# Kernel optimization log

Measured on AMD Instinct MI355X. Metric: run time of the kernel, lower is better.

## Reference

```python
import jax, jax.numpy as jnp
import numpy as np

D = 1024
N_A = 4096
N_V = 4096


def setup_inputs() -> dict:
    key = jax.random.key(0)
    ks = jax.random.split(key, 6)
    s = 1.0 / np.sqrt(D)  # like torch Linear default init scale
    return {
        "inputs_a": jax.random.normal(ks[0], (N_A, D), dtype=jnp.float32),
        "inputs_v": jax.random.normal(ks[1], (N_V, D), dtype=jnp.float32),
        "W_Ba": jax.random.uniform(ks[2], (D, D), jnp.float32, -s, s),
        "W_Aa": jax.random.uniform(ks[3], (D, D), jnp.float32, -s, s),
        "W_Bv": jax.random.uniform(ks[4], (D, D), jnp.float32, -s, s),
        "W_Av": jax.random.uniform(ks[5], (D, D), jnp.float32, -s, s),
    }


def reference(inputs_a, inputs_v, W_Ba, W_Aa, W_Bv, W_Av):
    # torch Linear: y = x @ W.T ; weights stored [out, in]
    a_a = inputs_a @ W_Aa.T                      # [N_a, D]
    b_a = inputs_a @ W_Ba.T                      # [N_a, D]
    a_v = inputs_v @ W_Av.T                      # [N_v, D]
    b_v = inputs_v @ W_Bv.T                      # [N_v, D]
    scores = b_a @ a_v.T                         # [N_a, N_v]
    alpha_av = jax.nn.softmax(scores, axis=1)    # softmax over N_v
    att_avv = alpha_av @ b_v                     # [N_a, D]
    att_vaa = alpha_av.T @ a_a                   # [N_v, D]
    feature_map_a = att_avv + inputs_a
    feature_map_v = att_vaa + inputs_v
    return feature_map_a, feature_map_v
```

## Files before the change

### kernel.cpp

```cpp
#include <hip/hip_runtime.h>
#include <stdint.h>

#define D_DIM 1024
#define NA_DIM 4096
#define NV_DIM 4096

typedef __bf16 bf16_t;
typedef __bf16 bf16x8 __attribute__((ext_vector_type(8)));
typedef float f32x4 __attribute__((ext_vector_type(4)));

__device__ __forceinline__ void gload_lds16(const void* g, void* lds) {
  __builtin_amdgcn_global_load_lds(
      (const __attribute__((address_space(1))) unsigned int*)g,
      (__attribute__((address_space(3))) unsigned int*)lds, 16, 0, 0);
}

#define VMW(N) asm volatile("s_waitcnt vmcnt(" #N ")" ::: "memory")
#define LKW(N) asm volatile("s_waitcnt lgkmcnt(" #N ")" ::: "memory")
#define SB0() __builtin_amdgcn_sched_barrier(0)
#define BAR() asm volatile("s_barrier" ::: "memory")

__device__ __forceinline__ void gemm256_pl(const bf16_t* __restrict__ A,
                                           const bf16_t* __restrict__ B,
                                           int K, int kb, int klen, int bm, int bn,
                                           bf16_t* lds, f32x4 acc[8][4]) {
  const int tid = threadIdx.x;
  const int lane = tid & 63;
  const int wid = tid >> 6;
  const int wm = wid >> 2;
  const int wn = wid & 3;
  const int frow = lane & 15;
  const int hi = lane >> 4;
  const int k0e = ((hi ^ (frow & 7)) << 3);

  const int sr = (wid << 4) + (lane >> 3);
  const int sc = (((lane & 7) ^ (lane >> 3)) << 3);
  const bf16_t* pAs = A + (size_t)(bm + sr) * K + kb + sc;
  const bf16_t* pBs = B + (size_t)(bn + sr) * K + kb + sc;
  const int dstW = wid << 10;

  const int aBase = (wm << 13) + frow * 64 + k0e;
  const int bBase = 16384 + ((wn >> 1) << 13) + ((wn & 1) << 12) + frow * 64 + k0e;

#define STG_A(kt, h, bufb) do { \
    const bf16_t* s_ = pAs + (size_t)((h) * 128) * K + (size_t)(kt) * 64; \
    bf16_t* d_ = lds + (bufb) * 32768 + (h) * 8192 + dstW; \
    gload_lds16(s_, d_); gload_lds16(s_ + (size_t)8 * K, d_ + 512); } while (0)
#define STG_B(kt, h, bufb) do { \
    const bf16_t* s_ = pBs + (size_t)((h) * 128) * K + (size_t)(kt) * 64; \
    bf16_t* d_ = lds + (bufb) * 32768 + 16384 + (h) * 8192 + dstW; \
    gload_lds16(s_, d_); gload_lds16(s_ + (size_t)8 * K, d_ + 512); } while (0)

  bf16x8 aF[2][4];
  bf16x8 bF[4][2];

#define READ_A(S, Q, BUFB) do { const bf16_t* Lb_ = lds + (BUFB) * 32768; \
    aF[S][0] = *(const bf16x8*)&Lb_[aBase + (Q) * 2048]; \
    aF[S][1] = *(const bf16x8*)&Lb_[(aBase ^ 32) + (Q) * 2048]; \
    aF[S][2] = *(const bf16x8*)&Lb_[aBase + (Q) * 2048 + 1024]; \
    aF[S][3] = *(const bf16x8*)&Lb_[(aBase ^ 32) + (Q) * 2048 + 1024]; } while (0)
#define READ_B(BUFB) do { const bf16_t* Lb_ = lds + (BUFB) * 32768; \
    _Pragma("unroll") for (int fc = 0; fc < 4; ++fc) { \
      bF[fc][0] = *(const bf16x8*)&Lb_[bBase + fc * 1024]; \
      bF[fc][1] = *(const bf16x8*)&Lb_[(bBase ^ 32) + fc * 1024]; } } while (0)

#define MFMA16(S, Q) do { \
    __builtin_amdgcn_s_setprio(1); \
    _Pragma("unroll") for (int fc = 0; fc < 4; ++fc) { \
      acc[(Q) * 2][fc]     = __builtin_amdgcn_mfma_f32_16x16x32_bf16(aF[S][0], bF[fc][0], acc[(Q) * 2][fc], 0, 0, 0); \
      acc[(Q) * 2][fc]     = __builtin_amdgcn_mfma_f32_16x16x32_bf16(aF[S][1], bF[fc][1], acc[(Q) * 2][fc], 0, 0, 0); \
      acc[(Q) * 2 + 1][fc] = __builtin_amdgcn_mfma_f32_16x16x32_bf16(aF[S][2], bF[fc][0], acc[(Q) * 2 + 1][fc], 0, 0, 0); \
      acc[(Q) * 2 + 1][fc] = __builtin_amdgcn_mfma_f32_16x16x32_bf16(aF[S][3], bF[fc][1], acc[(Q) * 2 + 1][fc], 0, 0, 0); \
    } \
    __builtin_amdgcn_s_setprio(0); } while (0)

#define TILE(P, T) do { \
    const bool mA = ((T) + 1 < NT); \
    const bool mB = ((T) + 2 < NT); \
     \
    READ_B(P); READ_A(0, 0, P); READ_A(1, 1, P); \
    if (mA) STG_A((T) + 1, 0, (P) ^ 1); \
    BAR(); LKW(4); SB0(); MFMA16(0, 0); BAR(); \
     \
    READ_A(0, 2, P); \
    if (mA) STG_A((T) + 1, 1, (P) ^ 1); \
    BAR(); LKW(4); SB0(); MFMA16(1, 1); BAR(); \
     \
    READ_A(1, 3, P); \
    if (mB) STG_B((T) + 2, 0, P); \
    BAR(); LKW(4); SB0(); MFMA16(0, 2); BAR(); \
     \
    if (mB) { STG_B((T) + 2, 1, P); VMW(4); } else { VMW(0); } \
    BAR(); LKW(0); SB0(); MFMA16(1, 3); BAR(); \
  } while (0)

  const int NT = klen >> 6;

  STG_B(0, 0, 0); STG_B(0, 1, 0); STG_A(0, 0, 0); STG_A(0, 1, 0);
  STG_B(1, 0, 1); STG_B(1, 1, 1);
  VMW(4);
  BAR();

  for (int it = 0; it < (NT >> 1); ++it) {
    TILE(0, 2 * it);
    TILE(1, 2 * it + 1);
  }
  VMW(0);
#undef TILE
#undef MFMA16
#undef READ_A
#undef READ_B
#undef STG_A
#undef STG_B
}

template <int BF16OUT>
__device__ __forceinline__ void store256(void* Cv, int ldc, int bm, int bn, f32x4 acc[8][4]) {
  const int lane = threadIdx.x & 63;
  const int wid = threadIdx.x >> 6;
  const int wm = wid >> 2, wn = wid & 3;
  const int frow = lane & 15, hi = lane >> 4;
  const int row0 = bm + wm * 128 + hi * 4;
  const int col0 = bn + wn * 64 + frow;
#pragma unroll
  for (int rf = 0; rf < 8; ++rf)
#pragma unroll
    for (int fc = 0; fc < 4; ++fc)
#pragma unroll
      for (int r = 0; r < 4; ++r) {
        size_t idx = (size_t)(row0 + rf * 16 + r) * ldc + (col0 + fc * 16);
        if constexpr (BF16OUT) ((bf16_t*)Cv)[idx] = (bf16_t)acc[rf][fc][r];
        else ((float*)Cv)[idx] = acc[rf][fc][r];
      }
}

__global__ __launch_bounds__(512, 1) void gemm_proj4(
    const bf16_t* __restrict__ Xa, const bf16_t* __restrict__ Xv,
    const bf16_t* __restrict__ W0, const bf16_t* __restrict__ W1,
    const bf16_t* __restrict__ W2, const bf16_t* __restrict__ W3,
    bf16_t* __restrict__ C0, bf16_t* __restrict__ C1,
    bf16_t* __restrict__ C2, bf16_t* __restrict__ C3) {
  __shared__ bf16_t lds[65536];
  const int z = blockIdx.z;
  const bf16_t* A = (z < 2) ? Xa : Xv;
  const bf16_t* B = (z == 0) ? W0 : (z == 1) ? W1 : (z == 2) ? W2 : W3;
  bf16_t* C = (z == 0) ? C0 : (z == 1) ? C1 : (z == 2) ? C2 : C3;
  f32x4 acc[8][4] = {};
  gemm256_pl(A, B, D_DIM, 0, D_DIM, blockIdx.x * 256, blockIdx.y * 256, lds, acc);
  store256<1>(C, D_DIM, blockIdx.x * 256, blockIdx.y * 256, acc);
}

__global__ __launch_bounds__(512, 1) void gemm_scores(const bf16_t* __restrict__ A,
                                                      const bf16_t* __restrict__ B,
                                                      float* __restrict__ C) {
  __shared__ bf16_t lds[65536];
  f32x4 acc[8][4] = {};
  gemm256_pl(A, B, D_DIM, 0, D_DIM, blockIdx.x * 256, blockIdx.y * 256, lds, acc);
  store256<0>(C, NV_DIM, blockIdx.x * 256, blockIdx.y * 256, acc);
}

__global__ __launch_bounds__(512, 1) void gemm_splitk(
    const bf16_t* __restrict__ alpha, const bf16_t* __restrict__ bvT,
    const bf16_t* __restrict__ alphaT, const bf16_t* __restrict__ aaT,
    float* __restrict__ P) {
  __shared__ bf16_t lds[65536];
  const int z = blockIdx.z;
  const bf16_t* A = (z < 2) ? alpha : alphaT;
  const bf16_t* B = (z < 2) ? bvT : aaT;
  const int kb = (z & 1) * 2048;
  f32x4 acc[8][4] = {};
  gemm256_pl(A, B, 4096, kb, 2048, blockIdx.x * 256, blockIdx.y * 256, lds, acc);
  store256<0>(P + (size_t)z * NA_DIM * D_DIM, D_DIM, blockIdx.x * 256, blockIdx.y * 256, acc);
}

__global__ __launch_bounds__(256) void reduce_splitk(const float* __restrict__ P,
                                                     const float* __restrict__ resA,
                                                     const float* __restrict__ resV,
                                                     float* __restrict__ out) {
  const int g = blockIdx.y;
  const size_t n = (size_t)NA_DIM * D_DIM;
  size_t i = ((size_t)blockIdx.x * 256 + threadIdx.x) * 4;
  const float* p0 = P + (size_t)g * 2 * n;
  const float* p1 = p0 + n;
  const float* r = g ? resV : resA;
  float4 a = *(const float4*)(p0 + i);
  float4 b = *(const float4*)(p1 + i);
  float4 c = *(const float4*)(r + i);
  float4 o = {a.x + b.x + c.x, a.y + b.y + c.y, a.z + b.z + c.z, a.w + b.w + c.w};
  *(float4*)(out + g * n + i) = o;
}

__device__ __forceinline__ void cvt8(const float* in, bf16_t* out, int i) {
  float4 v0 = *(const float4*)(in + i);
  float4 v1 = *(const float4*)(in + i + 4);
  bf16x8 o;
  o[0] = (bf16_t)v0.x; o[1] = (bf16_t)v0.y; o[2] = (bf16_t)v0.z; o[3] = (bf16_t)v0.w;
  o[4] = (bf16_t)v1.x; o[5] = (bf16_t)v1.y; o[6] = (bf16_t)v1.z; o[7] = (bf16_t)v1.w;
  *(bf16x8*)(out + i) = o;
}

__global__ __launch_bounds__(256) void cvt2(const float* __restrict__ inA,
                                            const float* __restrict__ inV,
                                            bf16_t* __restrict__ oA,
                                            bf16_t* __restrict__ oV) {
  const float* in = blockIdx.y ? inV : inA;
  bf16_t* out = blockIdx.y ? oV : oA;
  cvt8(in, out, (blockIdx.x * 256 + threadIdx.x) * 8);
}

__global__ __launch_bounds__(256) void cvt4(const float* __restrict__ i0, const float* __restrict__ i1,
                                            const float* __restrict__ i2, const float* __restrict__ i3,
                                            bf16_t* __restrict__ o0, bf16_t* __restrict__ o1,
                                            bf16_t* __restrict__ o2, bf16_t* __restrict__ o3) {
  const int z = blockIdx.y;
  const float* in = (z == 0) ? i0 : (z == 1) ? i1 : (z == 2) ? i2 : i3;
  bf16_t* out = (z == 0) ? o0 : (z == 1) ? o1 : (z == 2) ? o2 : o3;
  cvt8(in, out, (blockIdx.x * 256 + threadIdx.x) * 8);
}

__global__ __launch_bounds__(256) void softmax_rows(const float* __restrict__ S,
                                                    bf16_t* __restrict__ P) {
  const int row = blockIdx.x;
  const int ncol = 4096;
  const float* s = S + (size_t)row * ncol;
  const int base = threadIdx.x * 16;
  float v[16];
  float4* vp = (float4*)v;
#pragma unroll
  for (int q = 0; q < 4; ++q) vp[q] = *(const float4*)(s + base + q * 4);
  float m = v[0];
#pragma unroll
  for (int q = 1; q < 16; ++q) m = fmaxf(m, v[q]);
  for (int off = 32; off; off >>= 1) m = fmaxf(m, __shfl_xor(m, off));
  __shared__ float sm[4], ss[4];
  const int wid = threadIdx.x >> 6, lane = threadIdx.x & 63;
  if (lane == 0) sm[wid] = m;
  __syncthreads();
  m = fmaxf(fmaxf(sm[0], sm[1]), fmaxf(sm[2], sm[3]));
  float sum = 0.f;
#pragma unroll
  for (int q = 0; q < 16; ++q) { v[q] = __expf(v[q] - m); sum += v[q]; }
  for (int off = 32; off; off >>= 1) sum += __shfl_xor(sum, off);
  if (lane == 0) ss[wid] = sum;
  __syncthreads();
  const float inv = 1.0f / (ss[0] + ss[1] + ss[2] + ss[3]);
  bf16x8 o0, o1;
#pragma unroll
  for (int q = 0; q < 8; ++q) { o0[q] = (bf16_t)(v[q] * inv); o1[q] = (bf16_t)(v[q + 8] * inv); }
  bf16_t* p = P + (size_t)row * ncol + base;
  *(bf16x8*)p = o0;
  *(bf16x8*)(p + 8) = o1;
}

__global__ __launch_bounds__(256) void transpose_bf16(const bf16_t* __restrict__ in,
                                                      bf16_t* __restrict__ out, int R, int C) {
  __shared__ bf16_t t[64][72];
  const int bx = blockIdx.x * 64;
  const int by = blockIdx.y * 64;
  const int tid = threadIdx.x;
  const int c8 = (tid & 7) * 8;
  const int r = tid >> 3;
#pragma unroll
  for (int rr = 0; rr < 64; rr += 32) {
    bf16x8 v = *(const bf16x8*)(in + (size_t)(by + r + rr) * C + bx + c8);
    *(bf16x8*)&t[r + rr][c8] = v;
  }
  __syncthreads();
#pragma unroll
  for (int rr = 0; rr < 64; rr += 32) {
    bf16x8 v;
#pragma unroll
    for (int q = 0; q < 8; ++q) v[q] = t[c8 + q][r + rr];
    *(bf16x8*)(out + (size_t)(bx + r + rr) * R + by + c8) = v;
  }
}

extern "C" void kernel_launch(void* const* d_in, const int* in_sizes, int n_in,
                              void* d_out, int out_size, void* d_ws, size_t ws_size,
                              hipStream_t stream) {
  (void)in_sizes; (void)n_in; (void)out_size; (void)ws_size;
  const float* inA = (const float*)d_in[0];
  const float* inV = (const float*)d_in[1];
  const float* wBa = (const float*)d_in[2];
  const float* wAa = (const float*)d_in[3];
  const float* wBv = (const float*)d_in[4];
  const float* wAv = (const float*)d_in[5];
  float* out = (float*)d_out;

  char* w = (char*)d_ws;
  auto take = [&](size_t bytes) { void* p = (void*)w; w += bytes; return p; };
  const size_t XB = (size_t)NA_DIM * D_DIM * 2;
  const size_t WB = (size_t)D_DIM * D_DIM * 2;
  bf16_t* XaB = (bf16_t*)take(XB);
  bf16_t* XvB = (bf16_t*)take(XB);
  bf16_t* WBaB = (bf16_t*)take(WB);
  bf16_t* WAaB = (bf16_t*)take(WB);
  bf16_t* WBvB = (bf16_t*)take(WB);
  bf16_t* WAvB = (bf16_t*)take(WB);
  bf16_t* b_a = (bf16_t*)take(XB);
  bf16_t* a_v = (bf16_t*)take(XB);
  bf16_t* a_a = (bf16_t*)take(XB);
  bf16_t* b_v = (bf16_t*)take(XB);
  bf16_t* a_aT = (bf16_t*)take(XB);
  bf16_t* b_vT = (bf16_t*)take(XB);
  float* scores = (float*)take((size_t)NA_DIM * NV_DIM * 4);
  bf16_t* alpha = (bf16_t*)take((size_t)NA_DIM * NV_DIM * 2);
  bf16_t* alphaT = (bf16_t*)take((size_t)NA_DIM * NV_DIM * 2);
  float* P = scores;

  cvt2<<<dim3(NA_DIM * D_DIM / 2048, 2), 256, 0, stream>>>(inA, inV, XaB, XvB);
  cvt4<<<dim3(D_DIM * D_DIM / 2048, 4), 256, 0, stream>>>(wBa, wAa, wAv, wBv,
                                                          WBaB, WAaB, WAvB, WBvB);

  gemm_proj4<<<dim3(NA_DIM / 256, D_DIM / 256, 4), 512, 0, stream>>>(
      XaB, XvB, WBaB, WAaB, WAvB, WBvB, b_a, a_a, a_v, b_v);

  gemm_scores<<<dim3(NA_DIM / 256, NV_DIM / 256), 512, 0, stream>>>(b_a, a_v, scores);

  softmax_rows<<<NA_DIM, 256, 0, stream>>>(scores, alpha);

  transpose_bf16<<<dim3(NV_DIM / 64, NA_DIM / 64), 256, 0, stream>>>(alpha, alphaT, NA_DIM, NV_DIM);
  transpose_bf16<<<dim3(D_DIM / 64, NA_DIM / 64), 256, 0, stream>>>(a_a, a_aT, NA_DIM, D_DIM);
  transpose_bf16<<<dim3(D_DIM / 64, NV_DIM / 64), 256, 0, stream>>>(b_v, b_vT, NV_DIM, D_DIM);

  gemm_splitk<<<dim3(NA_DIM / 256, D_DIM / 256, 4), 512, 0, stream>>>(
      alpha, b_vT, alphaT, a_aT, P);
  reduce_splitk<<<dim3(NA_DIM * D_DIM / 1024, 2), 256, 0, stream>>>(P, inA, inV, out);
}
```

Before: 211.6 us.

## Replace hand-scheduled GEMM pipeline with simple double-buffered loop

Removes the hand-interleaved four-phase schedule with barriers, priority hints and sched_barriers in the shared GEMM mainloop. The new loop issues the next tile's A and B loads up front, then reads LDS fragments and runs the MFMAs, with a full wait and barrier at the end of each tile. It leaves instruction scheduling to the compiler and simplifies the code, at the cost of less fine-grained overlap between loads and math.

Measured after the change: 209.7 us. About the same (-0.9%).

```diff
diff --git a/kernel.cpp b/kernel.cpp
--- a/kernel.cpp
+++ b/kernel.cpp
@@ -17,13 +17,12 @@
 
 #define VMW(N) asm volatile("s_waitcnt vmcnt(" #N ")" ::: "memory")
 #define LKW(N) asm volatile("s_waitcnt lgkmcnt(" #N ")" ::: "memory")
-#define SB0() __builtin_amdgcn_sched_barrier(0)
 #define BAR() asm volatile("s_barrier" ::: "memory")
 
-__device__ __forceinline__ void gemm256_pl(const bf16_t* __restrict__ A,
-                                           const bf16_t* __restrict__ B,
-                                           int K, int kb, int klen, int bm, int bn,
-                                           bf16_t* lds, f32x4 acc[8][4]) {
+__device__ __forceinline__ void gemm256_loose(const bf16_t* __restrict__ A,
+                                              const bf16_t* __restrict__ B,
+                                              int K, int kb, int klen, int bm, int bn,
+                                              bf16_t* lds, f32x4 acc[8][4]) {
   const int tid = threadIdx.x;
   const int lane = tid & 63;
   const int wid = tid >> 6;
@@ -51,65 +50,48 @@
     bf16_t* d_ = lds + (bufb) * 32768 + 16384 + (h) * 8192 + dstW; \
     gload_lds16(s_, d_); gload_lds16(s_ + (size_t)8 * K, d_ + 512); } while (0)
 
-  bf16x8 aF[2][4];
-  bf16x8 bF[4][2];
-
-#define READ_A(S, Q, BUFB) do { const bf16_t* Lb_ = lds + (BUFB) * 32768; \
-    aF[S][0] = *(const bf16x8*)&Lb_[aBase + (Q) * 2048]; \
-    aF[S][1] = *(const bf16x8*)&Lb_[(aBase ^ 32) + (Q) * 2048]; \
-    aF[S][2] = *(const bf16x8*)&Lb_[aBase + (Q) * 2048 + 1024]; \
-    aF[S][3] = *(const bf16x8*)&Lb_[(aBase ^ 32) + (Q) * 2048 + 1024]; } while (0)
-#define READ_B(BUFB) do { const bf16_t* Lb_ = lds + (BUFB) * 32768; \
-    _Pragma("unroll") for (int fc = 0; fc < 4; ++fc) { \
-      bF[fc][0] = *(const bf16x8*)&Lb_[bBase + fc * 1024]; \
-      bF[fc][1] = *(const bf16x8*)&Lb_[(bBase ^ 32) + fc * 1024]; } } while (0)
-
-#define MFMA16(S, Q) do { \
-    __builtin_amdgcn_s_setprio(1); \
-    _Pragma("unroll") for (int fc = 0; fc < 4; ++fc) { \
-      acc[(Q) * 2][fc]     = __builtin_amdgcn_mfma_f32_16x16x32_bf16(aF[S][0], bF[fc][0], acc[(Q) * 2][fc], 0, 0, 0); \
-      acc[(Q) * 2][fc]     = __builtin_amdgcn_mfma_f32_16x16x32_bf16(aF[S][1], bF[fc][1], acc[(Q) * 2][fc], 0, 0, 0); \
-      acc[(Q) * 2 + 1][fc] = __builtin_amdgcn_mfma_f32_16x16x32_bf16(aF[S][2], bF[fc][0], acc[(Q) * 2 + 1][fc], 0, 0, 0); \
-      acc[(Q) * 2 + 1][fc] = __builtin_amdgcn_mfma_f32_16x16x32_bf16(aF[S][3], bF[fc][1], acc[(Q) * 2 + 1][fc], 0, 0, 0); \
+#define MFMA(a, b, c) __builtin_amdgcn_mfma_f32_16x16x32_bf16((a), (b), (c), 0, 0, 0)
+
+#define TILE(P, T) do { \
+    if ((T) + 1 < NT) { \
+      STG_A((T) + 1, 0, (P) ^ 1); STG_A((T) + 1, 1, (P) ^ 1); \
+      STG_B((T) + 1, 0, (P) ^ 1); STG_B((T) + 1, 1, (P) ^ 1); \
     } \
-    __builtin_amdgcn_s_setprio(0); } while (0)
-
-#define TILE(P, T) do { \
-    const bool mA = ((T) + 1 < NT); \
-    const bool mB = ((T) + 2 < NT); \
-     \
-    READ_B(P); READ_A(0, 0, P); READ_A(1, 1, P); \
-    if (mA) STG_A((T) + 1, 0, (P) ^ 1); \
-    BAR(); LKW(4); SB0(); MFMA16(0, 0); BAR(); \
-     \
-    READ_A(0, 2, P); \
-    if (mA) STG_A((T) + 1, 1, (P) ^ 1); \
-    BAR(); LKW(4); SB0(); MFMA16(1, 1); BAR(); \
-     \
-    READ_A(1, 3, P); \
-    if (mB) STG_B((T) + 2, 0, P); \
-    BAR(); LKW(4); SB0(); MFMA16(0, 2); BAR(); \
-     \
-    if (mB) { STG_B((T) + 2, 1, P); VMW(4); } else { VMW(0); } \
-    BAR(); LKW(0); SB0(); MFMA16(1, 3); BAR(); \
+    { \
+      const bf16_t* Lb_ = lds + (P) * 32768; \
+      bf16x8 bf0[4], bf1[4]; \
+      _Pragma("unroll") for (int fc = 0; fc < 4; ++fc) { \
+        bf0[fc] = *(const bf16x8*)&Lb_[bBase + fc * 1024]; \
+        bf1[fc] = *(const bf16x8*)&Lb_[(bBase ^ 32) + fc * 1024]; \
+      } \
+      _Pragma("unroll") for (int q = 0; q < 4; ++q) { \
+        bf16x8 a0 = *(const bf16x8*)&Lb_[aBase + q * 2048]; \
+        bf16x8 a1 = *(const bf16x8*)&Lb_[(aBase ^ 32) + q * 2048]; \
+        bf16x8 a2 = *(const bf16x8*)&Lb_[aBase + q * 2048 + 1024]; \
+        bf16x8 a3 = *(const bf16x8*)&Lb_[(aBase ^ 32) + q * 2048 + 1024]; \
+        _Pragma("unroll") for (int fc = 0; fc < 4; ++fc) { \
+          acc[q * 2][fc]     = MFMA(a0, bf0[fc], acc[q * 2][fc]); \
+          acc[q * 2][fc]     = MFMA(a1, bf1[fc], acc[q * 2][fc]); \
+          acc[q * 2 + 1][fc] = MFMA(a2, bf0[fc], acc[q * 2 + 1][fc]); \
+          acc[q * 2 + 1][fc] = MFMA(a3, bf1[fc], acc[q * 2 + 1][fc]); \
+        } \
+      } \
+    } \
+    LKW(0); VMW(0); BAR(); \
   } while (0)
 
   const int NT = klen >> 6;
 
-  STG_B(0, 0, 0); STG_B(0, 1, 0); STG_A(0, 0, 0); STG_A(0, 1, 0);
-  STG_B(1, 0, 1); STG_B(1, 1, 1);
-  VMW(4);
+  STG_A(0, 0, 0); STG_A(0, 1, 0); STG_B(0, 0, 0); STG_B(0, 1, 0);
+  VMW(0);
   BAR();
 
   for (int it = 0; it < (NT >> 1); ++it) {
     TILE(0, 2 * it);
     TILE(1, 2 * it + 1);
   }
-  VMW(0);
 #undef TILE
-#undef MFMA16
-#undef READ_A
-#undef READ_B
+#undef MFMA
 #undef STG_A
 #undef STG_B
 }
@@ -146,7 +128,7 @@
   const bf16_t* B = (z == 0) ? W0 : (z == 1) ? W1 : (z == 2) ? W2 : W3;
   bf16_t* C = (z == 0) ? C0 : (z == 1) ? C1 : (z == 2) ? C2 : C3;
   f32x4 acc[8][4] = {};
-  gemm256_pl(A, B, D_DIM, 0, D_DIM, blockIdx.x * 256, blockIdx.y * 256, lds, acc);
+  gemm256_loose(A, B, D_DIM, 0, D_DIM, blockIdx.x * 256, blockIdx.y * 256, lds, acc);
   store256<1>(C, D_DIM, blockIdx.x * 256, blockIdx.y * 256, acc);
 }
 
@@ -155,7 +137,7 @@
                                                       float* __restrict__ C) {
   __shared__ bf16_t lds[65536];
   f32x4 acc[8][4] = {};
-  gemm256_pl(A, B, D_DIM, 0, D_DIM, blockIdx.x * 256, blockIdx.y * 256, lds, acc);
+  gemm256_loose(A, B, D_DIM, 0, D_DIM, blockIdx.x * 256, blockIdx.y * 256, lds, acc);
   store256<0>(C, NV_DIM, blockIdx.x * 256, blockIdx.y * 256, acc);
 }
 
@@ -169,7 +151,7 @@
   const bf16_t* B = (z < 2) ? bvT : aaT;
   const int kb = (z & 1) * 2048;
   f32x4 acc[8][4] = {};
-  gemm256_pl(A, B, 4096, kb, 2048, blockIdx.x * 256, blockIdx.y * 256, lds, acc);
+  gemm256_loose(A, B, 4096, kb, 2048, blockIdx.x * 256, blockIdx.y * 256, lds, acc);
   store256<0>(P + (size_t)z * NA_DIM * D_DIM, D_DIM, blockIdx.x * 256, blockIdx.y * 256, acc);
 }
 
```
